# Kernel tuning notes

Measured on AMD Instinct MI355X. Metric: run time of the kernel, lower is better.

The kernel has to match this reference:

```python
import jax, jax.numpy as jnp
import numpy as np

HIDDEN = 2048
N_HEADS = 32
N_KV_HEADS = 8
HEAD_DIM = HIDDEN // N_HEADS  # 64
KV_DIM = N_KV_HEADS * HEAD_DIM  # 512


def setup_inputs() -> dict:
    key = jax.random.key(0)
    ks = jax.random.split(key, 9)
    s = 1.0 / np.sqrt(HIDDEN)
    x = jax.random.normal(ks[0], (2, 2048, HIDDEN), dtype=jnp.float32)
    wq = jax.random.uniform(ks[1], (HIDDEN, HIDDEN), jnp.float32, -s, s)
    bq = jax.random.uniform(ks[2], (HIDDEN,), jnp.float32, -s, s)
    wk = jax.random.uniform(ks[3], (KV_DIM, HIDDEN), jnp.float32, -s, s)
    bk = jax.random.uniform(ks[4], (KV_DIM,), jnp.float32, -s, s)
    wv = jax.random.uniform(ks[5], (KV_DIM, HIDDEN), jnp.float32, -s, s)
    bv = jax.random.uniform(ks[6], (KV_DIM,), jnp.float32, -s, s)
    wo = jax.random.uniform(ks[7], (HIDDEN, HIDDEN), jnp.float32, -s, s)
    bo = jax.random.uniform(ks[8], (HIDDEN,), jnp.float32, -s, s)
    return {"x": x, "wq": wq, "bq": bq, "wk": wk, "bk": bk,
            "wv": wv, "bv": bv, "wo": wo, "bo": bo}


def reference(x, wq, bq, wk, bk, wv, bv, wo, bo):
    B, S, _ = x.shape
    group = N_HEADS // N_KV_HEADS  # 4
    # projections (torch Linear: x @ W.T + b)
    q = (x @ wq.T + bq).reshape(B, S, N_HEADS, HEAD_DIM).transpose(0, 2, 1, 3)      # [B,H,S,D]
    k = (x @ wk.T + bk).reshape(B, S, N_KV_HEADS, HEAD_DIM).transpose(0, 2, 1, 3)   # [B,Hk,S,D]
    v = (x @ wv.T + bv).reshape(B, S, N_KV_HEADS, HEAD_DIM).transpose(0, 2, 1, 3)
    # repeat_interleave KV heads to match query heads
    k = jnp.repeat(k, group, axis=1)  # [B,H,S,D]
    v = jnp.repeat(v, group, axis=1)
    scale = 1.0 / np.sqrt(HEAD_DIM).astype(np.float32)
    attn = jnp.einsum('bhqd,bhkd->bhqk', q, k) * scale  # [B,H,S,S]
    score = jax.nn.softmax(attn, axis=-1)
    out = jnp.einsum('bhqk,bhkd->bhqd', score, v)       # [B,H,S,D]
    out = out.transpose(0, 2, 1, 3).reshape(B, S, HIDDEN)
    return out @ wo.T + bo
```

## Files before the change

kernel.cpp:

```cpp
#include <hip/hip_runtime.h>

typedef __attribute__((ext_vector_type(8))) short bf16x8;
typedef __attribute__((ext_vector_type(4))) float f32x4;
typedef __attribute__((ext_vector_type(16))) float f32x16;
typedef __attribute__((ext_vector_type(2))) float f32x2;

__device__ __forceinline__ short f2b(float f) {
  union { unsigned u; float f; } c;
  c.f = f;
  unsigned r = (c.u + 0x7FFFu + ((c.u >> 16) & 1u)) >> 16;
  return (short)r;
}

__device__ __forceinline__ int cvt_pk_bf16(float lo, float hi) {
  int r;
  asm("v_cvt_pk_bf16_f32 %0, %1, %2" : "=v"(r) : "v"(lo), "v"(hi));
  return r;
}

__device__ __forceinline__ void plswap(int& a, int& b) {
  asm("v_permlane32_swap_b32 %0, %1" : "+v"(a), "+v"(b));
}

__device__ __forceinline__ f32x2 pk_add(f32x2 a, f32x2 b) {
  f32x2 d;
  asm("v_pk_add_f32 %0, %1, %2" : "=v"(d) : "v"(a), "v"(b));
  return d;
}

__device__ __forceinline__ unsigned permb(unsigned s0, unsigned s1, unsigned sel) {
  unsigned d;
  asm("v_perm_b32 %0, %1, %2, %3" : "=v"(d) : "v"(s0), "v"(s1), "s"(sel));
  return d;
}

__device__ __forceinline__ void async16(const void* g, void* l) {
  __builtin_amdgcn_global_load_lds(
      (const __attribute__((address_space(1))) unsigned*)g,
      (__attribute__((address_space(3))) unsigned*)l, 16, 0, 0);
}

__global__ __launch_bounds__(256)
void conv_all(const float* __restrict__ x,  const float* __restrict__ wq,
              const float* __restrict__ wk, const float* __restrict__ wv,
              const float* __restrict__ wo, short* __restrict__ dst) {
  const size_t M = 1048576;
  size_t i = ((size_t)blockIdx.x * 256 + threadIdx.x) * 4;
  const float* src; size_t off;
  if (i < 8 * M)       { src = x;  off = 0; }
  else if (i < 12 * M) { src = wq; off = 8 * M; }
  else if (i < 13 * M) { src = wk; off = 12 * M; }
  else if (i < 14 * M) { src = wv; off = 13 * M; }
  else                 { src = wo; off = 14 * M; }
  float4 v = *(const float4*)(src + (i - off));
  short4 o;
  o.x = f2b(v.x); o.y = f2b(v.y); o.z = f2b(v.z); o.w = f2b(v.w);
  *(short4*)(dst + i) = o;
}

template <bool F32OUT>
__global__ __launch_bounds__(256)
void gemm_bt_bias(const short* __restrict__ A, const short* __restrict__ Bw,
                  const float* __restrict__ bias, void* __restrict__ Cv,
                  int M, int N, int K) {
  __shared__ short lsA[128 * 64];
  __shared__ short lsB[128 * 64];
  const int tid  = threadIdx.x;
  const int wave = tid >> 6, lane = tid & 63;
  const int l31  = lane & 31, hl = lane >> 5;
  const int GX  = gridDim.x;
  const int nwg = GX * gridDim.y;
  const int dd  = blockIdx.x + blockIdx.y * GX;
  const int logical = (dd & 7) * (nwg >> 3) + (dd >> 3);
  const int m0 = (logical / GX) * 128, n0 = (logical % GX) * 128;
  const int wm = (wave >> 1) * 64, wn = (wave & 1) * 64;

  f32x16 acc[2][2];
#pragma unroll
  for (int i = 0; i < 2; i++)
#pragma unroll
    for (int j = 0; j < 2; j++)
#pragma unroll
      for (int r = 0; r < 16; r++) acc[i][j][r] = 0.f;

  const int R  = tid >> 3;
  const int cs = tid & 7;
  const int gc = (cs ^ (R & 7)) << 3;
  const short* Arow[4]; const short* Brow[4];
#pragma unroll
  for (int b = 0; b < 4; b++) {
    Arow[b] = A  + (size_t)(m0 + R + 32 * b) * K + gc;
    Brow[b] = Bw + (size_t)(n0 + R + 32 * b) * K + gc;
  }
  const int ldst = R * 64 + cs * 8;

  for (int k0 = 0; k0 < K; k0 += 64) {
#pragma unroll
    for (int b = 0; b < 4; b++) {
      async16(Arow[b] + k0, lsA + ldst + b * 32 * 64);
      async16(Brow[b] + k0, lsB + ldst + b * 32 * 64);
    }
    __syncthreads();

    bf16x8 af[2][4], bfr[2][4];
#pragma unroll
    for (int i = 0; i < 2; i++) {
      const int Rr = wm + i * 32 + l31;
#pragma unroll
      for (int kq = 0; kq < 4; kq++) {
        const int c = kq * 2 + hl;
        af[i][kq] = *(const bf16x8*)(lsA + Rr * 64 + ((c ^ (Rr & 7)) << 3));
      }
    }
#pragma unroll
    for (int j = 0; j < 2; j++) {
      const int Sr = wn + j * 32 + l31;
#pragma unroll
      for (int kq = 0; kq < 4; kq++) {
        const int c = kq * 2 + hl;
        bfr[j][kq] = *(const bf16x8*)(lsB + Sr * 64 + ((c ^ (Sr & 7)) << 3));
      }
    }
#pragma unroll
    for (int kq = 0; kq < 4; kq++)
#pragma unroll
      for (int i = 0; i < 2; i++)
#pragma unroll
        for (int j = 0; j < 2; j++)
          acc[i][j] = __builtin_amdgcn_mfma_f32_32x32x16_bf16(
              af[i][kq], bfr[j][kq], acc[i][j], 0, 0, 0);
    __syncthreads();
  }

#pragma unroll
  for (int j = 0; j < 2; j++) {
    const int col = n0 + wn + j * 32 + l31;
    const float bb = bias[col];
#pragma unroll
    for (int i = 0; i < 2; i++) {
      const int rowb = m0 + wm + i * 32;
#pragma unroll
      for (int r = 0; r < 16; r++) {
        const int row = rowb + (r & 3) + 8 * (r >> 2) + 4 * hl;
        const float val = acc[i][j][r] + bb;
        if (F32OUT)
          ((float*)Cv)[(size_t)row * N + col] = val;
        else
          ((short*)Cv)[(size_t)row * N + col] = f2b(val);
      }
    }
  }
}

__global__ __launch_bounds__(256)
void gemm_qkv(const short* __restrict__ A, const short* __restrict__ Bw,
              const float* __restrict__ bq, const float* __restrict__ bk,
              const float* __restrict__ bv,
              short* __restrict__ Qo, short* __restrict__ Ko, short* __restrict__ Vo) {
  const int K = 2048;
  __shared__ short lsA[128 * 64];
  __shared__ short lsB[128 * 64];
  const int tid  = threadIdx.x;
  const int wave = tid >> 6, lane = tid & 63;
  const int l31  = lane & 31, hl = lane >> 5;
  const int GX  = gridDim.x;
  const int nwg = GX * gridDim.y;
  const int dd  = blockIdx.x + blockIdx.y * GX;
  const int logical = (dd & 7) * (nwg >> 3) + (dd >> 3);
  const int m0 = (logical / GX) * 128, n0 = (logical % GX) * 128;
  const int wm = (wave >> 1) * 64, wn = (wave & 1) * 64;

  f32x16 acc[2][2];
#pragma unroll
  for (int i = 0; i < 2; i++)
#pragma unroll
    for (int j = 0; j < 2; j++)
#pragma unroll
      for (int r = 0; r < 16; r++) acc[i][j][r] = 0.f;

  const int R  = tid >> 3;
  const int cs = tid & 7;
  const int gc = (cs ^ (R & 7)) << 3;
  const short* Arow[4]; const short* Brow[4];
#pragma unroll
  for (int b = 0; b < 4; b++) {
    Arow[b] = A  + (size_t)(m0 + R + 32 * b) * K + gc;
    Brow[b] = Bw + (size_t)(n0 + R + 32 * b) * K + gc;
  }
  const int ldst = R * 64 + cs * 8;

  for (int k0 = 0; k0 < K; k0 += 64) {
#pragma unroll
    for (int b = 0; b < 4; b++) {
      async16(Arow[b] + k0, lsA + ldst + b * 32 * 64);
      async16(Brow[b] + k0, lsB + ldst + b * 32 * 64);
    }
    __syncthreads();

    bf16x8 af[2][4], bfr[2][4];
#pragma unroll
    for (int i = 0; i < 2; i++) {
      const int Rr = wm + i * 32 + l31;
#pragma unroll
      for (int kq = 0; kq < 4; kq++) {
        const int c = kq * 2 + hl;
        af[i][kq] = *(const bf16x8*)(lsA + Rr * 64 + ((c ^ (Rr & 7)) << 3));
      }
    }
#pragma unroll
    for (int j = 0; j < 2; j++) {
      const int Sr = wn + j * 32 + l31;
#pragma unroll
      for (int kq = 0; kq < 4; kq++) {
        const int c = kq * 2 + hl;
        bfr[j][kq] = *(const bf16x8*)(lsB + Sr * 64 + ((c ^ (Sr & 7)) << 3));
      }
    }
#pragma unroll
    for (int kq = 0; kq < 4; kq++)
#pragma unroll
      for (int i = 0; i < 2; i++)
#pragma unroll
        for (int j = 0; j < 2; j++)
          acc[i][j] = __builtin_amdgcn_mfma_f32_32x32x16_bf16(
              af[i][kq], bfr[j][kq], acc[i][j], 0, 0, 0);
    __syncthreads();
  }

  short* base; int stride, coff; const float* bias;
  if (n0 < 2048)      { base = Qo; stride = 2048; bias = bq; coff = 0; }
  else if (n0 < 2560) { base = Ko; stride = 512;  bias = bk; coff = 2048; }
  else                { base = Vo; stride = 512;  bias = bv; coff = 2560; }
  const float qs = (n0 < 2048) ? 0.18033688011112043f : 1.0f;

#pragma unroll
  for (int j = 0; j < 2; j++) {
    const int lc = n0 + wn + j * 32 + l31 - coff;
    const float bb = bias[lc];
#pragma unroll
    for (int i = 0; i < 2; i++) {
      const int rowb = m0 + wm + i * 32;
#pragma unroll
      for (int r = 0; r < 16; r++) {
        const int row = rowb + (r & 3) + 8 * (r >> 2) + 4 * hl;
        base[(size_t)row * stride + lc] = f2b((acc[i][j][r] + bb) * qs);
      }
    }
  }
}

#define S_LEN 2048
#define HID   2048
#define KVD   512
#define ST    72

__global__ __launch_bounds__(256)
void gqa_flash(const short* __restrict__ Q, const short* __restrict__ Kb,
               const short* __restrict__ Vb, short* __restrict__ O) {
  __shared__ __align__(16) short lsK[64 * ST];
  __shared__ __align__(16) short lsVt[64 * ST];
  __shared__ float lsum[4][32];

  const int tid  = threadIdx.x;
  const int wave = tid >> 6, lane = tid & 63;
  const int l31  = lane & 31, hl = lane >> 5;

  const int d  = blockIdx.x + (blockIdx.y << 6);
  const int by = ((d & 7) << 1) | (d >> 9);
  const int qb = (d >> 3) & 63;
  const int b = by >> 3, kvh = by & 7;
  const int h = kvh * 4 + wave;
  const int q0 = qb * 32;

  const short* Qrow = Q + (size_t)(b * S_LEN + q0 + l31) * HID + h * 64 + hl * 8;
  bf16x8 qf[4];
#pragma unroll
  for (int f = 0; f < 4; f++) qf[f] = *(const bf16x8*)(Qrow + f * 16);

  f32x16 o0, o1;
#pragma unroll
  for (int i = 0; i < 16; i++) { o0[i] = 0.f; o1[i] = 0.f; }
  float lloc = 0.f;

  const short* Kp = Kb + (size_t)b * S_LEN * KVD + kvh * 64;
  const short* Vp = Vb + (size_t)b * S_LEN * KVD + kvh * 64;

  const int keyA = tid >> 3, chK = (tid & 7) * 8;
  const int kpV = tid & 31, dcV = (tid >> 5) * 8;

  bf16x8 kf0 = *(const bf16x8*)(Kp + (size_t)keyA * KVD + chK);
  bf16x8 kf1 = *(const bf16x8*)(Kp + (size_t)(keyA + 32) * KVD + chK);
  bf16x8 vf0 = *(const bf16x8*)(Vp + (size_t)(2 * kpV) * KVD + dcV);
  bf16x8 vf1 = *(const bf16x8*)(Vp + (size_t)(2 * kpV + 1) * KVD + dcV);

  for (int k0 = 0; k0 < S_LEN; k0 += 64) {
    *(bf16x8*)(lsK + keyA * ST + chK) = kf0;
    *(bf16x8*)(lsK + (keyA + 32) * ST + chK) = kf1;
    {
      const unsigned* u0 = (const unsigned*)&vf0;
      const unsigned* u1 = (const unsigned*)&vf1;
#pragma unroll
      for (int jw = 0; jw < 4; jw++) {
        unsigned lo = permb(u1[jw], u0[jw], 0x05040100u);
        unsigned hi = permb(u1[jw], u0[jw], 0x07060302u);
        *(unsigned*)(lsVt + (dcV + 2 * jw)     * ST + 2 * kpV) = lo;
        *(unsigned*)(lsVt + (dcV + 2 * jw + 1) * ST + 2 * kpV) = hi;
      }
    }
    __syncthreads();

    const int kn = (k0 + 64) & (S_LEN - 1);
    kf0 = *(const bf16x8*)(Kp + (size_t)(kn + keyA) * KVD + chK);
    kf1 = *(const bf16x8*)(Kp + (size_t)(kn + keyA + 32) * KVD + chK);
    vf0 = *(const bf16x8*)(Vp + (size_t)(kn + 2 * kpV) * KVD + dcV);
    vf1 = *(const bf16x8*)(Vp + (size_t)(kn + 2 * kpV + 1) * KVD + dcV);

    f32x16 s0, s1;
#pragma unroll
    for (int i = 0; i < 16; i++) { s0[i] = 0.f; s1[i] = 0.f; }
    __builtin_amdgcn_s_setprio(1);
#pragma unroll
    for (int f = 0; f < 4; f++) {
      bf16x8 ka = *(const bf16x8*)(lsK + l31 * ST + f * 16 + hl * 8);
      bf16x8 kb = *(const bf16x8*)(lsK + (32 + l31) * ST + f * 16 + hl * 8);
      s0 = __builtin_amdgcn_mfma_f32_32x32x16_bf16(ka, qf[f], s0, 0, 0, 0);
      s1 = __builtin_amdgcn_mfma_f32_32x32x16_bf16(kb, qf[f], s1, 0, 0, 0);
    }
    __builtin_amdgcn_s_setprio(0);

#pragma unroll
    for (int i = 0; i < 16; i++) {
      s0[i] = __builtin_amdgcn_exp2f(s0[i]);
      s1[i] = __builtin_amdgcn_exp2f(s1[i]);
    }
    {
      const f32x2* p0 = (const f32x2*)&s0;
      const f32x2* p1 = (const f32x2*)&s1;
      f32x2 t0 = pk_add(p0[0], p1[0]);
      f32x2 t1 = pk_add(p0[1], p1[1]);
      f32x2 t2 = pk_add(p0[2], p1[2]);
      f32x2 t3 = pk_add(p0[3], p1[3]);
      f32x2 t4 = pk_add(p0[4], p1[4]);
      f32x2 t5 = pk_add(p0[5], p1[5]);
      f32x2 t6 = pk_add(p0[6], p1[6]);
      f32x2 t7 = pk_add(p0[7], p1[7]);
      t0 = pk_add(t0, t4); t1 = pk_add(t1, t5);
      t2 = pk_add(t2, t6); t3 = pk_add(t3, t7);
      t0 = pk_add(t0, t2); t1 = pk_add(t1, t3);
      t0 = pk_add(t0, t1);
      lloc += t0.x + t0.y;
    }
    int P2[2][8];
#pragma unroll
    for (int qq = 0; qq < 8; qq++) {
      P2[0][qq] = cvt_pk_bf16(s0[2 * qq], s0[2 * qq + 1]);
      P2[1][qq] = cvt_pk_bf16(s1[2 * qq], s1[2 * qq + 1]);
    }

    __builtin_amdgcn_s_setprio(1);
#pragma unroll
    for (int t = 0; t < 4; t++) {
      const int j = t >> 1, b0 = (t & 1) * 4;
      int w0 = P2[j][b0 + 0], w2 = P2[j][b0 + 2];
      int w1 = P2[j][b0 + 1], w3 = P2[j][b0 + 3];
      plswap(w0, w2);
      plswap(w1, w3);
      union { unsigned u[4]; bf16x8 v; } pa;
      pa.u[0] = (unsigned)w0; pa.u[1] = (unsigned)w1;
      pa.u[2] = (unsigned)w2; pa.u[3] = (unsigned)w3;
      bf16x8 bv0 = *(const bf16x8*)(lsVt + l31 * ST + t * 16 + hl * 8);
      bf16x8 bv1 = *(const bf16x8*)(lsVt + (32 + l31) * ST + t * 16 + hl * 8);
      o0 = __builtin_amdgcn_mfma_f32_32x32x16_bf16(pa.v, bv0, o0, 0, 0, 0);
      o1 = __builtin_amdgcn_mfma_f32_32x32x16_bf16(pa.v, bv1, o1, 0, 0, 0);
    }
    __builtin_amdgcn_s_setprio(0);
    __builtin_amdgcn_sched_barrier(0);
    __builtin_amdgcn_s_barrier();
    __builtin_amdgcn_sched_barrier(0);
  }

  const float lfull = lloc + __shfl(lloc, lane ^ 32);
  if (lane < 32) lsum[wave][lane] = lfull;
#pragma unroll
  for (int r = 0; r < 16; r++) {
    const int qrow = (r & 3) + 8 * (r >> 2) + 4 * hl;
    const float rl = 1.0f / lsum[wave][qrow];
    short* op = O + (size_t)(b * S_LEN + q0 + qrow) * HID + h * 64 + l31;
    op[0]  = f2b(o0[r] * rl);
    op[32] = f2b(o1[r] * rl);
  }
}

extern "C" void kernel_launch(void* const* d_in, const int* in_sizes, int n_in,
                              void* d_out, int out_size, void* d_ws, size_t ws_size,
                              hipStream_t stream) {
  const float* x  = (const float*)d_in[0];
  const float* wq = (const float*)d_in[1];
  const float* bq = (const float*)d_in[2];
  const float* wk = (const float*)d_in[3];
  const float* bk = (const float*)d_in[4];
  const float* wv = (const float*)d_in[5];
  const float* bv = (const float*)d_in[6];
  const float* wo = (const float*)d_in[7];
  const float* bo = (const float*)d_in[8];
  float* out = (float*)d_out;

  short* xb  = (short*)d_ws;
  short* wqb = xb  + (size_t)4096 * 2048;
  short* wkb = wqb + (size_t)2048 * 2048;
  short* wvb = wkb + (size_t)512 * 2048;
  short* wob = wvb + (size_t)512 * 2048;
  short* Qb  = wob + (size_t)2048 * 2048;
  short* Kb  = Qb  + (size_t)4096 * 2048;
  short* Vb  = Kb  + (size_t)4096 * 512;
  short* AO  = Vb  + (size_t)4096 * 512;

  dim3 blk(256);
  conv_all<<<18 * 1048576 / 1024, blk, 0, stream>>>(x, wq, wk, wv, wo, xb);

  gemm_qkv<<<dim3(3072 / 128, 4096 / 128), blk, 0, stream>>>(xb, wqb, bq, bk, bv, Qb, Kb, Vb);
  gqa_flash<<<dim3(2048 / 32, 16), blk, 0, stream>>>(Qb, Kb, Vb, AO);
  gemm_bt_bias<true><<<dim3(2048 / 128, 4096 / 128), blk, 0, stream>>>(AO, wob, bo, out, 4096, 2048, 2048);
}
```

Baseline: 309.4 us.

## Process two 32-row query tiles per wave in flash attention

Each wave now handles 64 query rows (two 32-row tiles) instead of 32, so every K/V tile staged in shared memory is reused for twice as many queries. The grid is halved to 512 blocks and the block-index swizzle is adjusted to match. This cuts global and LDS K/V traffic and the number of barriers per query. The cost is roughly double the accumulator and Q-fragment registers, which may lower occupancy, and fewer blocks to spread across the CUs.

```diff
diff --git a/kernel.cpp b/kernel.cpp
--- a/kernel.cpp
+++ b/kernel.cpp
@@ -259,28 +259,35 @@
                const short* __restrict__ Vb, short* __restrict__ O) {
   __shared__ __align__(16) short lsK[64 * ST];
   __shared__ __align__(16) short lsVt[64 * ST];
-  __shared__ float lsum[4][32];
+  __shared__ float lsum[4][64];
 
   const int tid  = threadIdx.x;
   const int wave = tid >> 6, lane = tid & 63;
   const int l31  = lane & 31, hl = lane >> 5;
 
-  const int d  = blockIdx.x + (blockIdx.y << 6);
-  const int by = ((d & 7) << 1) | (d >> 9);
-  const int qb = (d >> 3) & 63;
+  const int d  = blockIdx.x + (blockIdx.y << 5);
+  const int by = ((d & 7) << 1) | (d >> 8);
+  const int qb = (d >> 3) & 31;
   const int b = by >> 3, kvh = by & 7;
   const int h = kvh * 4 + wave;
-  const int q0 = qb * 32;
-
-  const short* Qrow = Q + (size_t)(b * S_LEN + q0 + l31) * HID + h * 64 + hl * 8;
-  bf16x8 qf[4];
-#pragma unroll
-  for (int f = 0; f < 4; f++) qf[f] = *(const bf16x8*)(Qrow + f * 16);
-
-  f32x16 o0, o1;
-#pragma unroll
-  for (int i = 0; i < 16; i++) { o0[i] = 0.f; o1[i] = 0.f; }
-  float lloc = 0.f;
+  const int q0 = qb * 64;
+
+  bf16x8 qf[2][4];
+#pragma unroll
+  for (int qt = 0; qt < 2; qt++)
+#pragma unroll
+    for (int f = 0; f < 4; f++)
+      qf[qt][f] = *(const bf16x8*)(Q + (size_t)(b * S_LEN + q0 + qt * 32 + l31) * HID +
+                                   h * 64 + f * 16 + hl * 8);
+
+  f32x16 o[2][2];
+#pragma unroll
+  for (int qt = 0; qt < 2; qt++)
+#pragma unroll
+    for (int j = 0; j < 2; j++)
+#pragma unroll
+      for (int i = 0; i < 16; i++) o[qt][j][i] = 0.f;
+  float lloc0 = 0.f, lloc1 = 0.f;
 
   const short* Kp = Kb + (size_t)b * S_LEN * KVD + kvh * 64;
   const short* Vp = Vb + (size_t)b * S_LEN * KVD + kvh * 64;
@@ -315,80 +322,91 @@
     vf0 = *(const bf16x8*)(Vp + (size_t)(kn + 2 * kpV) * KVD + dcV);
     vf1 = *(const bf16x8*)(Vp + (size_t)(kn + 2 * kpV + 1) * KVD + dcV);
 
-    f32x16 s0, s1;
-#pragma unroll
-    for (int i = 0; i < 16; i++) { s0[i] = 0.f; s1[i] = 0.f; }
-    __builtin_amdgcn_s_setprio(1);
-#pragma unroll
-    for (int f = 0; f < 4; f++) {
-      bf16x8 ka = *(const bf16x8*)(lsK + l31 * ST + f * 16 + hl * 8);
-      bf16x8 kb = *(const bf16x8*)(lsK + (32 + l31) * ST + f * 16 + hl * 8);
-      s0 = __builtin_amdgcn_mfma_f32_32x32x16_bf16(ka, qf[f], s0, 0, 0, 0);
-      s1 = __builtin_amdgcn_mfma_f32_32x32x16_bf16(kb, qf[f], s1, 0, 0, 0);
-    }
-    __builtin_amdgcn_s_setprio(0);
-
-#pragma unroll
-    for (int i = 0; i < 16; i++) {
-      s0[i] = __builtin_amdgcn_exp2f(s0[i]);
-      s1[i] = __builtin_amdgcn_exp2f(s1[i]);
-    }
-    {
-      const f32x2* p0 = (const f32x2*)&s0;
-      const f32x2* p1 = (const f32x2*)&s1;
-      f32x2 t0 = pk_add(p0[0], p1[0]);
-      f32x2 t1 = pk_add(p0[1], p1[1]);
-      f32x2 t2 = pk_add(p0[2], p1[2]);
-      f32x2 t3 = pk_add(p0[3], p1[3]);
-      f32x2 t4 = pk_add(p0[4], p1[4]);
-      f32x2 t5 = pk_add(p0[5], p1[5]);
-      f32x2 t6 = pk_add(p0[6], p1[6]);
-      f32x2 t7 = pk_add(p0[7], p1[7]);
-      t0 = pk_add(t0, t4); t1 = pk_add(t1, t5);
-      t2 = pk_add(t2, t6); t3 = pk_add(t3, t7);
-      t0 = pk_add(t0, t2); t1 = pk_add(t1, t3);
-      t0 = pk_add(t0, t1);
-      lloc += t0.x + t0.y;
-    }
-    int P2[2][8];
-#pragma unroll
-    for (int qq = 0; qq < 8; qq++) {
-      P2[0][qq] = cvt_pk_bf16(s0[2 * qq], s0[2 * qq + 1]);
-      P2[1][qq] = cvt_pk_bf16(s1[2 * qq], s1[2 * qq + 1]);
-    }
-
-    __builtin_amdgcn_s_setprio(1);
-#pragma unroll
-    for (int t = 0; t < 4; t++) {
-      const int j = t >> 1, b0 = (t & 1) * 4;
-      int w0 = P2[j][b0 + 0], w2 = P2[j][b0 + 2];
-      int w1 = P2[j][b0 + 1], w3 = P2[j][b0 + 3];
-      plswap(w0, w2);
-      plswap(w1, w3);
-      union { unsigned u[4]; bf16x8 v; } pa;
-      pa.u[0] = (unsigned)w0; pa.u[1] = (unsigned)w1;
-      pa.u[2] = (unsigned)w2; pa.u[3] = (unsigned)w3;
-      bf16x8 bv0 = *(const bf16x8*)(lsVt + l31 * ST + t * 16 + hl * 8);
-      bf16x8 bv1 = *(const bf16x8*)(lsVt + (32 + l31) * ST + t * 16 + hl * 8);
-      o0 = __builtin_amdgcn_mfma_f32_32x32x16_bf16(pa.v, bv0, o0, 0, 0, 0);
-      o1 = __builtin_amdgcn_mfma_f32_32x32x16_bf16(pa.v, bv1, o1, 0, 0, 0);
-    }
-    __builtin_amdgcn_s_setprio(0);
+#pragma unroll
+    for (int qt = 0; qt < 2; qt++) {
+      f32x16 s0, s1;
+#pragma unroll
+      for (int i = 0; i < 16; i++) { s0[i] = 0.f; s1[i] = 0.f; }
+      __builtin_amdgcn_s_setprio(1);
+#pragma unroll
+      for (int f = 0; f < 4; f++) {
+        bf16x8 ka = *(const bf16x8*)(lsK + l31 * ST + f * 16 + hl * 8);
+        bf16x8 kb = *(const bf16x8*)(lsK + (32 + l31) * ST + f * 16 + hl * 8);
+        s0 = __builtin_amdgcn_mfma_f32_32x32x16_bf16(ka, qf[qt][f], s0, 0, 0, 0);
+        s1 = __builtin_amdgcn_mfma_f32_32x32x16_bf16(kb, qf[qt][f], s1, 0, 0, 0);
+      }
+      __builtin_amdgcn_s_setprio(0);
+
+#pragma unroll
+      for (int i = 0; i < 16; i++) {
+        s0[i] = __builtin_amdgcn_exp2f(s0[i]);
+        s1[i] = __builtin_amdgcn_exp2f(s1[i]);
+      }
+      {
+        const f32x2* p0 = (const f32x2*)&s0;
+        const f32x2* p1 = (const f32x2*)&s1;
+        f32x2 t0 = pk_add(p0[0], p1[0]);
+        f32x2 t1 = pk_add(p0[1], p1[1]);
+        f32x2 t2 = pk_add(p0[2], p1[2]);
+        f32x2 t3 = pk_add(p0[3], p1[3]);
+        f32x2 t4 = pk_add(p0[4], p1[4]);
+        f32x2 t5 = pk_add(p0[5], p1[5]);
+        f32x2 t6 = pk_add(p0[6], p1[6]);
+        f32x2 t7 = pk_add(p0[7], p1[7]);
+        t0 = pk_add(t0, t4); t1 = pk_add(t1, t5);
+        t2 = pk_add(t2, t6); t3 = pk_add(t3, t7);
+        t0 = pk_add(t0, t2); t1 = pk_add(t1, t3);
+        t0 = pk_add(t0, t1);
+        if (qt == 0) lloc0 += t0.x + t0.y; else lloc1 += t0.x + t0.y;
+      }
+      int P2[2][8];
+#pragma unroll
+      for (int qq = 0; qq < 8; qq++) {
+        P2[0][qq] = cvt_pk_bf16(s0[2 * qq], s0[2 * qq + 1]);
+        P2[1][qq] = cvt_pk_bf16(s1[2 * qq], s1[2 * qq + 1]);
+      }
+
+      __builtin_amdgcn_s_setprio(1);
+#pragma unroll
+      for (int t = 0; t < 4; t++) {
+        const int j = t >> 1, b0 = (t & 1) * 4;
+        int w0 = P2[j][b0 + 0], w2 = P2[j][b0 + 2];
+        int w1 = P2[j][b0 + 1], w3 = P2[j][b0 + 3];
+        plswap(w0, w2);
+        plswap(w1, w3);
+        union { unsigned u[4]; bf16x8 v; } pa;
+        pa.u[0] = (unsigned)w0; pa.u[1] = (unsigned)w1;
+        pa.u[2] = (unsigned)w2; pa.u[3] = (unsigned)w3;
+        bf16x8 bv0 = *(const bf16x8*)(lsVt + l31 * ST + t * 16 + hl * 8);
+        bf16x8 bv1 = *(const bf16x8*)(lsVt + (32 + l31) * ST + t * 16 + hl * 8);
+        o[qt][0] = __builtin_amdgcn_mfma_f32_32x32x16_bf16(pa.v, bv0, o[qt][0], 0, 0, 0);
+        o[qt][1] = __builtin_amdgcn_mfma_f32_32x32x16_bf16(pa.v, bv1, o[qt][1], 0, 0, 0);
+      }
+      __builtin_amdgcn_s_setprio(0);
+    }
     __builtin_amdgcn_sched_barrier(0);
     __builtin_amdgcn_s_barrier();
     __builtin_amdgcn_sched_barrier(0);
   }
 
-  const float lfull = lloc + __shfl(lloc, lane ^ 32);
-  if (lane < 32) lsum[wave][lane] = lfull;
-#pragma unroll
-  for (int r = 0; r < 16; r++) {
-    const int qrow = (r & 3) + 8 * (r >> 2) + 4 * hl;
-    const float rl = 1.0f / lsum[wave][qrow];
-    short* op = O + (size_t)(b * S_LEN + q0 + qrow) * HID + h * 64 + l31;
-    op[0]  = f2b(o0[r] * rl);
-    op[32] = f2b(o1[r] * rl);
-  }
+  {
+    const float lf0 = lloc0 + __shfl(lloc0, lane ^ 32);
+    const float lf1 = lloc1 + __shfl(lloc1, lane ^ 32);
+    if (lane < 32) {
+      lsum[wave][lane]      = lf0;
+      lsum[wave][32 + lane] = lf1;
+    }
+  }
+#pragma unroll
+  for (int qt = 0; qt < 2; qt++)
+#pragma unroll
+    for (int r = 0; r < 16; r++) {
+      const int qrow = qt * 32 + (r & 3) + 8 * (r >> 2) + 4 * hl;
+      const float rl = 1.0f / lsum[wave][qrow];
+      short* op = O + (size_t)(b * S_LEN + q0 + qrow) * HID + h * 64 + l31;
+      op[0]  = f2b(o[qt][0][r] * rl);
+      op[32] = f2b(o[qt][1][r] * rl);
+    }
 }
 
 extern "C" void kernel_launch(void* const* d_in, const int* in_sizes, int n_in,
@@ -419,6 +437,6 @@
   conv_all<<<18 * 1048576 / 1024, blk, 0, stream>>>(x, wq, wk, wv, wo, xb);
 
   gemm_qkv<<<dim3(3072 / 128, 4096 / 128), blk, 0, stream>>>(xb, wqb, bq, bk, bv, Qb, Kb, Vb);
-  gqa_flash<<<dim3(2048 / 32, 16), blk, 0, stream>>>(Qb, Kb, Vb, AO);
+  gqa_flash<<<dim3(2048 / 64, 16), blk, 0, stream>>>(Qb, Kb, Vb, AO);
   gemm_bt_bias<true><<<dim3(2048 / 128, 4096 / 128), blk, 0, stream>>>(AO, wob, bo, out, 4096, 2048, 2048);
 }
```

Measured after the change: 312.4 us. About the same (+0.9%).
